# Performance work log

Hardware: AMD Instinct MI355X
Metric: run time of the kernel (lower is better)

## Reference

```python
import math
import jax, jax.numpy as jnp
import numpy as np

NL, D, H, V, L = 6, 512, 8, 32000, 512
DK = D // H
PAD = 1


def _ln(x, g, b, eps=1e-6):
    mu = jnp.mean(x, -1, keepdims=True)
    var = jnp.mean((x - mu) ** 2, -1, keepdims=True)
    return (x - mu) * jax.lax.rsqrt(var + eps) * g + b


def _mha(xq, xkv, w, b, mask):
    # w: [4, D, D] (q, k, v, out), b: [4, D]; mask True = disallowed
    B, Tq, _ = xq.shape
    Tk = xkv.shape[1]
    q = (xq @ w[0] + b[0]).reshape(B, Tq, H, DK).transpose(0, 2, 1, 3)
    k = (xkv @ w[1] + b[1]).reshape(B, Tk, H, DK).transpose(0, 2, 1, 3)
    v = (xkv @ w[2] + b[2]).reshape(B, Tk, H, DK).transpose(0, 2, 1, 3)
    s = jnp.einsum('bhqd,bhkd->bhqk', q, k) / math.sqrt(DK)
    s = jnp.where(mask, -jnp.inf, s)
    a = jax.nn.softmax(s, -1)
    o = jnp.einsum('bhqk,bhkd->bhqd', a, v).transpose(0, 2, 1, 3).reshape(B, Tq, D)
    return o @ w[3] + b[3]


def _ffn(x, w1, b1, w2, b2):
    return jnp.maximum(x @ w1 + b1, 0.0) @ w2 + b2


def _forward(src, tgt, tok_emb, pos_emb, enc_attn_w, enc_attn_b, enc_ffn_w1, enc_ffn_b1,
             enc_ffn_w2, enc_ffn_b2, enc_ln, enc_fln, dec_attn_w, dec_attn_b,
             dec_ffn_w1, dec_ffn_b1, dec_ffn_w2, dec_ffn_b2, dec_ln, dec_fln):
    B, S = src.shape
    T = tgt.shape[1]
    src_mask = (src == PAD)[:, None, None, :]                    # [B,1,1,S]
    causal = ~jnp.tril(jnp.ones((T, T), bool))
    trg_mask = causal[None, None] | (tgt == PAD)[:, None, None, :]  # [B,1,T,T]

    # ----- encoder (pre-LN sublayers with residual) -----
    x = tok_emb[src] + pos_emb[jnp.arange(S)]
    for i in range(NL):
        h = _ln(x, enc_ln[i, 0, 0], enc_ln[i, 0, 1])
        x = x + _mha(h, h, enc_attn_w[i], enc_attn_b[i], src_mask)
        h = _ln(x, enc_ln[i, 1, 0], enc_ln[i, 1, 1])
        x = x + _ffn(h, enc_ffn_w1[i], enc_ffn_b1[i], enc_ffn_w2[i], enc_ffn_b2[i])
    mem = _ln(x, enc_fln[0], enc_fln[1])

    # ----- decoder -----
    y = tok_emb[tgt] + pos_emb[jnp.arange(T)]
    for i in range(NL):
        h = _ln(y, dec_ln[i, 0, 0], dec_ln[i, 0, 1])
        y = y + _mha(h, h, dec_attn_w[i, :4], dec_attn_b[i, :4], trg_mask)
        h = _ln(y, dec_ln[i, 1, 0], dec_ln[i, 1, 1])
        y = y + _mha(h, mem, dec_attn_w[i, 4:], dec_attn_b[i, 4:], src_mask)
        h = _ln(y, dec_ln[i, 2, 0], dec_ln[i, 2, 1])
        y = y + _ffn(h, dec_ffn_w1[i], dec_ffn_b1[i], dec_ffn_w2[i], dec_ffn_b2[i])
    y = _ln(y, dec_fln[0], dec_fln[1])

    # Generator: tied-weight projection + log_softmax
    logits = y @ tok_emb.T                                       # [B,T,V]
    return jax.nn.log_softmax(logits, -1)


def setup_inputs() -> dict:
    key = jax.random.key(0)
    ks = jax.random.split(key, 12)
    n = lambda k, shape, s=0.02: jax.random.normal(k, shape, jnp.float32) * s
    B, S, T = 8, 128, 128
    ln2 = jnp.tile(jnp.stack([jnp.ones(D), jnp.zeros(D)])[None, None], (NL, 2, 1, 1))
    ln3 = jnp.tile(jnp.stack([jnp.ones(D), jnp.zeros(D)])[None, None], (NL, 3, 1, 1))
    fln = jnp.stack([jnp.ones(D), jnp.zeros(D)])
    return {
        'src': jax.random.randint(ks[0], (B, S), 2, V),
        'tgt': jax.random.randint(ks[1], (B, T), 2, V),
        'tok_emb': n(ks[2], (V, D)),
        'pos_emb': n(ks[3], (L, D)),
        'enc_attn_w': n(ks[4], (NL, 4, D, D)),
        'enc_attn_b': jnp.zeros((NL, 4, D)),
        'enc_ffn_w1': n(ks[5], (NL, D, 4 * D)),
        'enc_ffn_b1': jnp.zeros((NL, 4 * D)),
        'enc_ffn_w2': n(ks[6], (NL, 4 * D, D)),
        'enc_ffn_b2': jnp.zeros((NL, D)),
        'enc_ln': ln2,
        'enc_fln': fln,
        'dec_attn_w': n(ks[7], (NL, 8, D, D)),
        'dec_attn_b': jnp.zeros((NL, 8, D)),
        'dec_ffn_w1': n(ks[8], (NL, D, 4 * D)),
        'dec_ffn_b1': jnp.zeros((NL, 4 * D)),
        'dec_ffn_w2': n(ks[9], (NL, 4 * D, D)),
        'dec_ffn_b2': jnp.zeros((NL, D)),
        'dec_ln': ln3,
        'dec_fln': fln,
    }


def reference(src, tgt, tok_emb, pos_emb, enc_attn_w, enc_attn_b, enc_ffn_w1, enc_ffn_b1,
              enc_ffn_w2, enc_ffn_b2, enc_ln, enc_fln, dec_attn_w, dec_attn_b,
              dec_ffn_w1, dec_ffn_b1, dec_ffn_w2, dec_ffn_b2, dec_ln, dec_fln):
    return _forward(src, tgt, tok_emb, pos_emb, enc_attn_w, enc_attn_b, enc_ffn_w1,
                    enc_ffn_b1, enc_ffn_w2, enc_ffn_b2, enc_ln, enc_fln, dec_attn_w,
                    dec_attn_b, dec_ffn_w1, dec_ffn_b1, dec_ffn_w2, dec_ffn_b2,
                    dec_ln, dec_fln)
```

## Files before the change

### kernel.cpp

```cpp
#include <hip/hip_runtime.h>
#include <hip/hip_bf16.h>

typedef unsigned short u16;
typedef unsigned int u32;
typedef __attribute__((ext_vector_type(8))) short bf8_t;
typedef __attribute__((ext_vector_type(4))) float f4_t;

#define D 512
#define H 8
#define DK 64
#define NL 6
#define V 32000
#define FF 2048
#define B 8
#define S 128
#define NTOK (B * S)

static __device__ inline u16 f2bs(float x) {
    __hip_bfloat16 h = __float2bfloat16(x);
    return *reinterpret_cast<u16*>(&h);
}
static __device__ inline float blo(u32 u) { return __uint_as_float(u << 16); }
static __device__ inline float bhi(u32 u) { return __uint_as_float(u & 0xffff0000u); }
static __device__ inline u32 pk2(float a, float b) {
    return ((u32)f2bs(b) << 16) | f2bs(a);
}

__global__ __launch_bounds__(256) void wconv_t(const float* __restrict__ in,
                                               u16* __restrict__ out,
                                               int R, int C)
{
    __shared__ u16 T[32][40];
    const float* inz = in + (size_t)blockIdx.z * R * C;
    u16* outz = out + (size_t)blockIdx.z * R * C;
    int r0 = blockIdx.y * 32, c0 = blockIdx.x * 32;
    int tid = threadIdx.x;
    {
        int r = tid >> 3, c4 = (tid & 7) * 4;
        float4 f = *(const float4*)&inz[(size_t)(r0 + r) * C + c0 + c4];
        T[c4 + 0][r] = f2bs(f.x);
        T[c4 + 1][r] = f2bs(f.y);
        T[c4 + 2][r] = f2bs(f.z);
        T[c4 + 3][r] = f2bs(f.w);
    }
    __syncthreads();
    {
        int c = tid >> 3, r4 = (tid & 7) * 4;
        u32 lo = ((u32)T[c][r4 + 1] << 16) | T[c][r4 + 0];
        u32 hi = ((u32)T[c][r4 + 3] << 16) | T[c][r4 + 2];
        uint2 p; p.x = lo; p.y = hi;
        *(uint2*)&outz[(size_t)(c0 + c) * R + r0 + r4] = p;
    }
}

__global__ __launch_bounds__(256) void ec_kernel(const float* __restrict__ in,
                                                 u16* __restrict__ out)
{
    size_t i = ((size_t)blockIdx.x * 256 + threadIdx.x) * 4;
    float4 f = *(const float4*)&in[i];
    uint2 p;
    p.x = pk2(f.x, f.y);
    p.y = pk2(f.z, f.w);
    *(uint2*)&out[i] = p;
}

__global__ __launch_bounds__(256) void embed2_kernel(
    const int* __restrict__ src, const int* __restrict__ tgt,
    const float* __restrict__ tok, const float* __restrict__ pos,
    float* __restrict__ xe, float* __restrict__ xd)
{
    int row = blockIdx.x;
    const int* ids; float* X; int r;
    if (row < NTOK) { ids = src; X = xe; r = row; }
    else            { ids = tgt; X = xd; r = row - NTOK; }
    int s  = r & (S - 1);
    int id = ids[r];
    int d  = threadIdx.x * 2;
    float2 t = *(const float2*)&tok[(size_t)id * D + d];
    float2 p = *(const float2*)&pos[(size_t)s * D + d];
    float2 o; o.x = t.x + p.x; o.y = t.y + p.y;
    *(float2*)&X[(size_t)r * D + d] = o;
}

__global__ void ln_kernel(const float* __restrict__ X,
                          const float* __restrict__ g,
                          const float* __restrict__ bta,
                          u16* __restrict__ Y)
{
    int row  = blockIdx.x;
    int lane = threadIdx.x;
    float v[8];
    float sum = 0.f;
#pragma unroll
    for (int i = 0; i < 8; ++i) {
        v[i] = X[row * D + i * 64 + lane];
        sum += v[i];
    }
#pragma unroll
    for (int off = 32; off > 0; off >>= 1) sum += __shfl_xor(sum, off);
    float mu = sum * (1.f / D);
    float var = 0.f;
#pragma unroll
    for (int i = 0; i < 8; ++i) { float d = v[i] - mu; var += d * d; }
#pragma unroll
    for (int off = 32; off > 0; off >>= 1) var += __shfl_xor(var, off);
    var *= (1.f / D);
    float r = rsqrtf(var + 1e-6f);
#pragma unroll
    for (int i = 0; i < 8; ++i) {
        int d = i * 64 + lane;
        Y[row * D + d] = f2bs((v[i] - mu) * r * g[d] + bta[d]);
    }
}

template<int MT, int KC, int LNA>
__global__ __launch_bounds__(256) void gk(
    const u16* __restrict__ Abf, const float* __restrict__ Axf,
    const float* __restrict__ g, const float* __restrict__ be,
    const u16* __restrict__ Bt, const float* __restrict__ bias,
    const float* __restrict__ resid, void* __restrict__ Cout,
    int K, int N, int relu, int obf, int swz,
    long wzs, long bzs, long ozs)
{
    constexpr int THREADS = 256;
    constexpr int SL = KC / 8;
    constexpr int NA = MT * SL / THREADS;
    constexpr int NB = 64 * SL / THREADS;
    constexpr int NJ = (MT == 32) ? 2 : 4;
    constexpr int TPR = THREADS / MT;
    __shared__ __align__(16) u16 As[MT][KC + 8];
    __shared__ __align__(16) u16 Bs[64][KC + 8];
    __shared__ float muS[MT], rsS[MT];
    __shared__ float gS[LNA ? D : 4], beS[LNA ? D : 4];

    int tid = threadIdx.x;
    int col0, row0, z;
    if (swz) {
        int id = blockIdx.x;
        int s = id & 7, t = id >> 3;
        int r = t & 15, q = t >> 4;
        int c = q * 8 + s;
        if (c >= 500) return;
        col0 = c * 64; row0 = r * MT; z = 0;
    } else {
        col0 = blockIdx.x * 64; row0 = blockIdx.y * MT; z = blockIdx.z;
    }

    const float* bz = bias ? bias + (size_t)z * bzs : nullptr;
    const u16* Bz = Bt + (size_t)z * wzs;

    int wv  = tid >> 6, ln = tid & 63;
    int m16 = ln & 15, quad = ln >> 4;
    int rb  = (MT == 32) ? (wv & 1) * 16 : wv * 16;
    int cb  = (MT == 32) ? (wv >> 1) * 32 : 0;

    bf8_t  pA[LNA ? 1 : NA];
    float4 pAf[LNA ? 2 * NA : 1];
    bf8_t  pB[NB];

    auto loadA = [&](int kc) {
#pragma unroll
        for (int i = 0; i < NA; ++i) {
            int idx = tid + i * THREADS;
            int m = idx / SL, s8 = (idx % SL) * 8;
            if constexpr (LNA) {
                const float* sp = &Axf[(size_t)(row0 + m) * D + kc + s8];
                pAf[2 * i]     = *(const float4*)sp;
                pAf[2 * i + 1] = *(const float4*)(sp + 4);
            } else {
                pA[i] = *(const bf8_t*)&Abf[(size_t)(row0 + m) * K + kc + s8];
            }
        }
    };
    auto loadB = [&](int kc) {
#pragma unroll
        for (int i = 0; i < NB; ++i) {
            int idx = tid + i * THREADS;
            int n = idx / SL, s8 = (idx % SL) * 8;
            pB[i] = *(const bf8_t*)&Bz[(size_t)(col0 + n) * K + kc + s8];
        }
    };
    auto writeLDS = [&](int kc) {
#pragma unroll
        for (int i = 0; i < NA; ++i) {
            int idx = tid + i * THREADS;
            int m = idx / SL, s8 = (idx % SL) * 8;
            if constexpr (LNA) {
                float mu = muS[m], rs = rsS[m];
                float4 f0 = pAf[2 * i], f1 = pAf[2 * i + 1];
                float4 g0 = *(const float4*)&gS[kc + s8];
                float4 g1 = *(const float4*)&gS[kc + s8 + 4];
                float4 b0 = *(const float4*)&beS[kc + s8];
                float4 b1 = *(const float4*)&beS[kc + s8 + 4];
                uint4 o;
                o.x = pk2((f0.x - mu) * rs * g0.x + b0.x, (f0.y - mu) * rs * g0.y + b0.y);
                o.y = pk2((f0.z - mu) * rs * g0.z + b0.z, (f0.w - mu) * rs * g0.w + b0.w);
                o.z = pk2((f1.x - mu) * rs * g1.x + b1.x, (f1.y - mu) * rs * g1.y + b1.y);
                o.w = pk2((f1.z - mu) * rs * g1.z + b1.z, (f1.w - mu) * rs * g1.w + b1.w);
                *(uint4*)&As[m][s8] = o;
            } else {
                *(bf8_t*)&As[m][s8] = pA[i];
            }
        }
#pragma unroll
        for (int i = 0; i < NB; ++i) {
            int idx = tid + i * THREADS;
            int n = idx / SL, s8 = (idx % SL) * 8;
            *(bf8_t*)&Bs[n][s8] = pB[i];
        }
    };

    loadA(0);
    loadB(0);
    if constexpr (LNA) {
        if (tid < 128) *(float4*)&gS[tid * 4] = *(const float4*)&g[tid * 4];
        else           *(float4*)&beS[(tid - 128) * 4] = *(const float4*)&be[(tid - 128) * 4];
        int r = tid / TPR, sR = tid % TPR;
        const float* xr = Axf + (size_t)(row0 + r) * D;
        float sum = 0.f, ss = 0.f;
#pragma unroll
        for (int c = 0; c < D / (TPR * 4); ++c) {
            float4 f = *(const float4*)&xr[c * TPR * 4 + sR * 4];
            sum += f.x + f.y + f.z + f.w;
            ss  += f.x * f.x + f.y * f.y + f.z * f.z + f.w * f.w;
        }
#pragma unroll
        for (int o = 1; o < TPR; o <<= 1) {
            sum += __shfl_xor(sum, o);
            ss  += __shfl_xor(ss, o);
        }
        if (sR == 0) {
            float mu  = sum * (1.f / D);
            float var = ss * (1.f / D) - mu * mu;
            muS[r] = mu;
            rsS[r] = rsqrtf(var + 1e-6f);
        }
        __syncthreads();
    }

    f4_t acc[NJ];
#pragma unroll
    for (int j = 0; j < NJ; ++j) acc[j] = (f4_t){0.f, 0.f, 0.f, 0.f};

    for (int kc = 0; kc < K; kc += KC) {
        writeLDS(kc);
        __syncthreads();
        if (kc + KC < K) { loadA(kc + KC); loadB(kc + KC); }
#pragma unroll
        for (int ks = 0; ks < KC / 32; ++ks) {
            bf8_t a = *(const bf8_t*)&As[rb + m16][ks * 32 + quad * 8];
#pragma unroll
            for (int j = 0; j < NJ; ++j) {
                bf8_t b = *(const bf8_t*)&Bs[cb + j * 16 + m16][ks * 32 + quad * 8];
                acc[j] = __builtin_amdgcn_mfma_f32_16x16x32_bf16(a, b, acc[j], 0, 0, 0);
            }
        }
        __syncthreads();
    }

#pragma unroll
    for (int j = 0; j < NJ; ++j) {
        int col = col0 + cb + j * 16 + m16;
        float bv = bz ? bz[col] : 0.f;
#pragma unroll
        for (int r = 0; r < 4; ++r) {
            int row = row0 + rb + quad * 4 + r;
            float val = acc[j][r] + bv;
            if (resid) val += resid[(size_t)row * N + col];
            if (relu) val = fmaxf(val, 0.f);
            if (obf) ((u16*)Cout + (size_t)z * ozs)[(size_t)row * N + col] = f2bs(val);
            else     ((float*)Cout + (size_t)z * ozs)[(size_t)row * N + col] = val;
        }
    }
}

__global__ __launch_bounds__(256) void attn_kernel(
    const u16* __restrict__ Qb, const u16* __restrict__ Kb,
    const u16* __restrict__ Vb, u16* __restrict__ Ob,
    const int* __restrict__ mask_ids, int causal)
{
    __shared__ u16 Ks[128][66];
    __shared__ u32 Vp[128][36];
    __shared__ u16 Qs[32][66];
    __shared__ float es[4][132];

    int qc = blockIdx.x;
    int h  = blockIdx.y;
    int b  = blockIdx.z;
    int tid = threadIdx.x;

    for (int i = tid; i < 1024; i += 256) {
        int t = i >> 3, d8 = (i & 7) * 8;
        size_t src = (size_t)(b * S + t) * D + h * DK + d8;
        uint4 kv = *(const uint4*)&Kb[src];
        *(u32*)&Ks[t][d8 + 0] = kv.x;
        *(u32*)&Ks[t][d8 + 2] = kv.y;
        *(u32*)&Ks[t][d8 + 4] = kv.z;
        *(u32*)&Ks[t][d8 + 6] = kv.w;
        uint4 vv = *(const uint4*)&Vb[src];
        *(uint4*)&Vp[t][d8 >> 1] = vv;
    }
    {
        int m = tid >> 3, d8 = (tid & 7) * 8;
        uint4 qv = *(const uint4*)&Qb[(size_t)(b * S + qc * 32 + m) * D + h * DK + d8];
        *(u32*)&Qs[m][d8 + 0] = qv.x;
        *(u32*)&Qs[m][d8 + 2] = qv.y;
        *(u32*)&Qs[m][d8 + 4] = qv.z;
        *(u32*)&Qs[m][d8 + 6] = qv.w;
    }
    __syncthreads();

    int w      = tid >> 6;
    int lane   = tid & 63;
    int d2     = lane & 31;
    int th     = lane >> 5;
    bool pad0  = (mask_ids[b * S + lane] == 1);
    bool pad1  = (mask_ids[b * S + 64 + lane] == 1);

    for (int qi = 0; qi < 8; ++qi) {
        int qloc = w * 8 + qi;
        int qpos = qc * 32 + qloc;

        float s0 = 0.f, s1 = 0.f;
#pragma unroll
        for (int i = 0; i < 32; ++i) {
            u32 qu = *(const u32*)&Qs[qloc][2 * i];
            u32 k0 = *(const u32*)&Ks[lane][2 * i];
            u32 k1 = *(const u32*)&Ks[lane + 64][2 * i];
            float ql = blo(qu), qh = bhi(qu);
            s0 += ql * blo(k0) + qh * bhi(k0);
            s1 += ql * blo(k1) + qh * bhi(k1);
        }
        s0 *= 0.125f; s1 *= 0.125f;
        if (pad0 || (causal && lane > qpos))        s0 = -1e30f;
        if (pad1 || (causal && (lane + 64) > qpos)) s1 = -1e30f;

        float mx = fmaxf(s0, s1);
#pragma unroll
        for (int off = 32; off > 0; off >>= 1) mx = fmaxf(mx, __shfl_xor(mx, off));
        float e0 = __expf(s0 - mx), e1 = __expf(s1 - mx);
        float l = e0 + e1;
#pragma unroll
        for (int off = 32; off > 0; off >>= 1) l += __shfl_xor(l, off);
        float inv = 1.f / l;
        es[w][lane]      = e0 * inv;
        es[w][lane + 64] = e1 * inv;

        float o0 = 0.f, o1 = 0.f;
#pragma unroll 8
        for (int i = 0; i < 64; ++i) {
            int t = th * 64 + i;
            float e = es[w][t];
            u32 vu = Vp[t][d2];
            o0 += e * blo(vu);
            o1 += e * bhi(vu);
        }
        o0 += __shfl_xor(o0, 32);
        o1 += __shfl_xor(o1, 32);
        if (th == 0) {
            u32 packed = ((u32)f2bs(o1) << 16) | f2bs(o0);
            *(u32*)&Ob[(size_t)(b * S + qpos) * D + h * DK + 2 * d2] = packed;
        }
    }
}

__global__ __launch_bounds__(256) void lsm_kernel(float* __restrict__ out)
{
    __shared__ float red[8];
    int row = blockIdx.x, tid = threadIdx.x;
    float* rp = out + (size_t)row * V;
    float v[125];
    float m = -1e30f;
#pragma unroll
    for (int i = 0; i < 125; ++i) {
        v[i] = rp[i * 256 + tid];
        m = fmaxf(m, v[i]);
    }
#pragma unroll
    for (int off = 32; off > 0; off >>= 1) m = fmaxf(m, __shfl_xor(m, off));
    int wv = tid >> 6;
    if ((tid & 63) == 0) red[wv] = m;
    __syncthreads();
    m = fmaxf(fmaxf(red[0], red[1]), fmaxf(red[2], red[3]));
    float l = 0.f;
#pragma unroll
    for (int i = 0; i < 125; ++i) l += __expf(v[i] - m);
#pragma unroll
    for (int off = 32; off > 0; off >>= 1) l += __shfl_xor(l, off);
    if ((tid & 63) == 0) red[4 + wv] = l;
    __syncthreads();
    l = (red[4] + red[5]) + (red[6] + red[7]);
    float c = m + logf(l);
#pragma unroll
    for (int i = 0; i < 125; ++i) rp[i * 256 + tid] = v[i] - c;
}

extern "C" void kernel_launch(void* const* d_in, const int* in_sizes, int n_in,
                              void* d_out, int out_size, void* d_ws, size_t ws_size,
                              hipStream_t stream)
{
    const int*   src        = (const int*)d_in[0];
    const int*   tgt        = (const int*)d_in[1];
    const float* tok_emb    = (const float*)d_in[2];
    const float* pos_emb    = (const float*)d_in[3];
    const float* enc_attn_w = (const float*)d_in[4];
    const float* enc_attn_b = (const float*)d_in[5];
    const float* enc_ffn_w1 = (const float*)d_in[6];
    const float* enc_ffn_b1 = (const float*)d_in[7];
    const float* enc_ffn_w2 = (const float*)d_in[8];
    const float* enc_ffn_b2 = (const float*)d_in[9];
    const float* enc_ln     = (const float*)d_in[10];
    const float* enc_fln    = (const float*)d_in[11];
    const float* dec_attn_w = (const float*)d_in[12];
    const float* dec_attn_b = (const float*)d_in[13];
    const float* dec_ffn_w1 = (const float*)d_in[14];
    const float* dec_ffn_b1 = (const float*)d_in[15];
    const float* dec_ffn_w2 = (const float*)d_in[16];
    const float* dec_ffn_b2 = (const float*)d_in[17];
    const float* dec_ln     = (const float*)d_in[18];
    const float* dec_fln    = (const float*)d_in[19];
    float* out = (float*)d_out;

    const size_t TOKD = (size_t)NTOK * D;
    const size_t DD   = (size_t)D * D;
    const size_t DF   = (size_t)D * FF;

    char* p = (char*)d_ws;
    auto carve = [&](size_t bytes) {
        void* r = (void*)p;
        p += (bytes + 255) & ~(size_t)255;
        return r;
    };
    u16* wtEA  = (u16*)carve(24 * DD * 2);
    u16* wtEF1 = (u16*)carve(6 * DF * 2);
    u16* wtEF2 = (u16*)carve(6 * DF * 2);
    u16* wtDA  = (u16*)carve(48 * DD * 2);
    u16* wtDF1 = (u16*)carve(6 * DF * 2);
    u16* wtDF2 = (u16*)carve(6 * DF * 2);
    u16* emb16 = (u16*)carve((size_t)V * D * 2);
    float* xe  = (float*)carve(TOKD * 4);
    float* xd  = (float*)carve(TOKD * 4);
    u16* h16   = (u16*)carve(TOKD * 2);
    u16* q16   = (u16*)carve(TOKD * 2 * 3);
    u16* k16   = q16 + TOKD;
    u16* v16   = k16 + TOKD;
    u16* ao16  = (u16*)carve(TOKD * 2);
    u16* mem16 = (u16*)carve(TOKD * 2);
    u16* mid16 = (u16*)carve((size_t)NTOK * FF * 2);
    u16* kc16  = (u16*)carve(6 * TOKD * 2);
    u16* vc16  = (u16*)carve(6 * TOKD * 2);

    dim3 b256(256), b64(64);
    dim3 gQKV(8, 32, 3);
    dim3 gP  (8, 32, 1);
    dim3 gKV6(8, 32, 6);
    dim3 gF1 (32, 16, 1);
    dim3 gF2 (8, 32, 1);
    dim3 gGen(8064, 1, 1);
    dim3 gAttn(4, H, B);

    wconv_t<<<dim3(16, 16, 24), b256, 0, stream>>>(enc_attn_w, wtEA, 512, 512);
    wconv_t<<<dim3(64, 16, 6),  b256, 0, stream>>>(enc_ffn_w1, wtEF1, 512, 2048);
    wconv_t<<<dim3(16, 64, 6),  b256, 0, stream>>>(enc_ffn_w2, wtEF2, 2048, 512);
    wconv_t<<<dim3(16, 16, 48), b256, 0, stream>>>(dec_attn_w, wtDA, 512, 512);
    wconv_t<<<dim3(64, 16, 6),  b256, 0, stream>>>(dec_ffn_w1, wtDF1, 512, 2048);
    wconv_t<<<dim3(16, 64, 6),  b256, 0, stream>>>(dec_ffn_w2, wtDF2, 2048, 512);
    ec_kernel<<<16000, b256, 0, stream>>>(tok_emb, emb16);

    embed2_kernel<<<2 * NTOK, b256, 0, stream>>>(src, tgt, tok_emb, pos_emb, xe, xd);

    for (int i = 0; i < NL; ++i) {
        const float* bb  = enc_attn_b + (size_t)i * 4 * D;
        const float* ln0 = enc_ln + (size_t)((i * 2 + 0) * 2) * D;
        const float* ln1 = enc_ln + (size_t)((i * 2 + 1) * 2) * D;

        gk<32, 128, 1><<<gQKV, b256, 0, stream>>>(nullptr, xe, ln0, ln0 + D,
            wtEA + (size_t)i * 4 * DD, bb, nullptr, q16,
            512, 512, 0, 1, 0, (long)DD, (long)D, (long)TOKD);
        attn_kernel<<<gAttn, b256, 0, stream>>>(q16, k16, v16, ao16, src, 0);
        gk<32, 128, 0><<<gP, b256, 0, stream>>>(ao16, nullptr, nullptr, nullptr,
            wtEA + (size_t)(i * 4 + 3) * DD, bb + 3 * D, xe, xe,
            512, 512, 0, 0, 0, 0, 0, 0);
        gk<64, 128, 1><<<gF1, b256, 0, stream>>>(nullptr, xe, ln1, ln1 + D,
            wtEF1 + (size_t)i * DF, enc_ffn_b1 + (size_t)i * FF, nullptr, mid16,
            512, 2048, 1, 1, 0, 0, 0, 0);
        gk<32, 128, 0><<<gF2, b256, 0, stream>>>(mid16, nullptr, nullptr, nullptr,
            wtEF2 + (size_t)i * DF, enc_ffn_b2 + (size_t)i * D, xe, xe,
            2048, 512, 0, 0, 0, 0, 0, 0);
    }
    ln_kernel<<<NTOK, b64, 0, stream>>>(xe, enc_fln, enc_fln + D, mem16);

    gk<32, 128, 0><<<gKV6, b256, 0, stream>>>(mem16, nullptr, nullptr, nullptr,
        wtDA + 5 * DD, dec_attn_b + 5 * D, nullptr, kc16,
        512, 512, 0, 1, 0, (long)(8 * DD), (long)(8 * D), (long)TOKD);
    gk<32, 128, 0><<<gKV6, b256, 0, stream>>>(mem16, nullptr, nullptr, nullptr,
        wtDA + 6 * DD, dec_attn_b + 6 * D, nullptr, vc16,
        512, 512, 0, 1, 0, (long)(8 * DD), (long)(8 * D), (long)TOKD);

    for (int i = 0; i < NL; ++i) {
        const float* bb  = dec_attn_b + (size_t)i * 8 * D;
        const u16*   wt  = wtDA + (size_t)i * 8 * DD;
        const float* ln0 = dec_ln + (size_t)((i * 3 + 0) * 2) * D;
        const float* ln1 = dec_ln + (size_t)((i * 3 + 1) * 2) * D;
        const float* ln2 = dec_ln + (size_t)((i * 3 + 2) * 2) * D;

        gk<32, 128, 1><<<gQKV, b256, 0, stream>>>(nullptr, xd, ln0, ln0 + D,
            wt, bb, nullptr, q16,
            512, 512, 0, 1, 0, (long)DD, (long)D, (long)TOKD);
        attn_kernel<<<gAttn, b256, 0, stream>>>(q16, k16, v16, ao16, tgt, 1);
        gk<32, 128, 0><<<gP, b256, 0, stream>>>(ao16, nullptr, nullptr, nullptr,
            wt + 3 * DD, bb + 3 * D, xd, xd,
            512, 512, 0, 0, 0, 0, 0, 0);

        gk<32, 128, 1><<<gP, b256, 0, stream>>>(nullptr, xd, ln1, ln1 + D,
            wt + 4 * DD, bb + 4 * D, nullptr, q16,
            512, 512, 0, 1, 0, 0, 0, 0);
        attn_kernel<<<gAttn, b256, 0, stream>>>(q16, kc16 + (size_t)i * TOKD,
            vc16 + (size_t)i * TOKD, ao16, src, 0);
        gk<32, 128, 0><<<gP, b256, 0, stream>>>(ao16, nullptr, nullptr, nullptr,
            wt + 7 * DD, bb + 7 * D, xd, xd,
            512, 512, 0, 0, 0, 0, 0, 0);

        gk<64, 128, 1><<<gF1, b256, 0, stream>>>(nullptr, xd, ln2, ln2 + D,
            wtDF1 + (size_t)i * DF, dec_ffn_b1 + (size_t)i * FF, nullptr, mid16,
            512, 2048, 1, 1, 0, 0, 0, 0);
        gk<32, 128, 0><<<gF2, b256, 0, stream>>>(mid16, nullptr, nullptr, nullptr,
            wtDF2 + (size_t)i * DF, dec_ffn_b2 + (size_t)i * D, xd, xd,
            2048, 512, 0, 0, 0, 0, 0, 0);
    }
    ln_kernel<<<NTOK, b64, 0, stream>>>(xd, dec_fln, dec_fln + D, h16);

    gk<64, 128, 0><<<gGen, b256, 0, stream>>>(h16, nullptr, nullptr, nullptr,
        emb16, nullptr, nullptr, out,
        512, V, 0, 0, 1, 0, 0, 0);
    lsm_kernel<<<NTOK, b256, 0, stream>>>(out);
}
```

Baseline: 1.687 ms.

## Fuse LN+QKV projection into attention, merge prep kernels, stage fp32 epilogue

Merges the six weight-conversion launches, embedding cast and embed kernels into one prep launch. Replaces the separate LN+QKV GEMM and attention kernels with fused kernels (fqa for self-attention, fca for cross-attention) that compute per-head Q/K/V in LDS and run attention directly, so the q/k/v tensors never go through global memory. Adds an LDS-staged, float4-coalesced fp32 epilogue to the GEMM and changes the generator GEMM K-chunk from 128 to 64. The fused kernels recompute K/V for every query-chunk block (4x redundant projection work) and use 512-thread blocks with large shared memory, which can lower occupancy.

Measured after the change: 1.600 ms. 1.05x faster.

```diff
diff --git a/kernel.cpp b/kernel.cpp
--- a/kernel.cpp
+++ b/kernel.cpp
@@ -26,15 +26,13 @@
     return ((u32)f2bs(b) << 16) | f2bs(a);
 }
 
-__global__ __launch_bounds__(256) void wconv_t(const float* __restrict__ in,
-                                               u16* __restrict__ out,
-                                               int R, int C)
+__device__ inline void wconv_body(const float* __restrict__ in, u16* __restrict__ out,
+                                  int R, int C, int bx, int by, int bz, int tid,
+                                  u16 (*T)[40])
 {
-    __shared__ u16 T[32][40];
-    const float* inz = in + (size_t)blockIdx.z * R * C;
-    u16* outz = out + (size_t)blockIdx.z * R * C;
-    int r0 = blockIdx.y * 32, c0 = blockIdx.x * 32;
-    int tid = threadIdx.x;
+    const float* inz = in + (size_t)bz * R * C;
+    u16* outz = out + (size_t)bz * R * C;
+    int r0 = by * 32, c0 = bx * 32;
     {
         int r = tid >> 3, c4 = (tid & 7) * 4;
         float4 f = *(const float4*)&inz[(size_t)(r0 + r) * C + c0 + c4];
@@ -53,33 +51,52 @@
     }
 }
 
-__global__ __launch_bounds__(256) void ec_kernel(const float* __restrict__ in,
-                                                 u16* __restrict__ out)
+__global__ __launch_bounds__(256) void prep(
+    const float* __restrict__ eaw, const float* __restrict__ ef1,
+    const float* __restrict__ ef2, const float* __restrict__ daw,
+    const float* __restrict__ df1, const float* __restrict__ df2,
+    u16* __restrict__ wEA, u16* __restrict__ wEF1, u16* __restrict__ wEF2,
+    u16* __restrict__ wDA, u16* __restrict__ wDF1, u16* __restrict__ wDF2,
+    const float* __restrict__ tok, u16* __restrict__ emb16,
+    const int* __restrict__ src, const int* __restrict__ tgt,
+    const float* __restrict__ pos, float* __restrict__ xe, float* __restrict__ xd)
 {
-    size_t i = ((size_t)blockIdx.x * 256 + threadIdx.x) * 4;
-    float4 f = *(const float4*)&in[i];
-    uint2 p;
-    p.x = pk2(f.x, f.y);
-    p.y = pk2(f.z, f.w);
-    *(uint2*)&out[i] = p;
-}
-
-__global__ __launch_bounds__(256) void embed2_kernel(
-    const int* __restrict__ src, const int* __restrict__ tgt,
-    const float* __restrict__ tok, const float* __restrict__ pos,
-    float* __restrict__ xe, float* __restrict__ xd)
-{
-    int row = blockIdx.x;
-    const int* ids; float* X; int r;
-    if (row < NTOK) { ids = src; X = xe; r = row; }
-    else            { ids = tgt; X = xd; r = row - NTOK; }
-    int s  = r & (S - 1);
-    int id = ids[r];
-    int d  = threadIdx.x * 2;
-    float2 t = *(const float2*)&tok[(size_t)id * D + d];
-    float2 p = *(const float2*)&pos[(size_t)s * D + d];
-    float2 o; o.x = t.x + p.x; o.y = t.y + p.y;
-    *(float2*)&X[(size_t)r * D + d] = o;
+    __shared__ u16 T[32][40];
+    int id = blockIdx.x, tid = threadIdx.x;
+    if (id < 6144)  { wconv_body(eaw, wEA, 512, 512,  id % 16, (id / 16) % 16, id / 256,  tid, T); return; }
+    id -= 6144;
+    if (id < 6144)  { wconv_body(ef1, wEF1, 512, 2048, id % 64, (id / 64) % 16, id / 1024, tid, T); return; }
+    id -= 6144;
+    if (id < 6144)  { wconv_body(ef2, wEF2, 2048, 512, id % 16, (id / 16) % 64, id / 1024, tid, T); return; }
+    id -= 6144;
+    if (id < 12288) { wconv_body(daw, wDA, 512, 512,  id % 16, (id / 16) % 16, id / 256,  tid, T); return; }
+    id -= 12288;
+    if (id < 6144)  { wconv_body(df1, wDF1, 512, 2048, id % 64, (id / 64) % 16, id / 1024, tid, T); return; }
+    id -= 6144;
+    if (id < 6144)  { wconv_body(df2, wDF2, 2048, 512, id % 16, (id / 16) % 64, id / 1024, tid, T); return; }
+    id -= 6144;
+    if (id < 16000) {
+        size_t i = ((size_t)id * 256 + tid) * 4;
+        float4 f = *(const float4*)&tok[i];
+        uint2 p;
+        p.x = pk2(f.x, f.y);
+        p.y = pk2(f.z, f.w);
+        *(uint2*)&emb16[i] = p;
+        return;
+    }
+    id -= 16000;
+    {
+        const int* ids; float* X; int r;
+        if (id < NTOK) { ids = src; X = xe; r = id; }
+        else           { ids = tgt; X = xd; r = id - NTOK; }
+        int s  = r & (S - 1);
+        int tk = ids[r];
+        int d  = tid * 2;
+        float2 t = *(const float2*)&tok[(size_t)tk * D + d];
+        float2 p = *(const float2*)&pos[(size_t)s * D + d];
+        float2 o; o.x = t.x + p.x; o.y = t.y + p.y;
+        *(float2*)&X[(size_t)r * D + d] = o;
+    }
 }
 
 __global__ void ln_kernel(const float* __restrict__ X,
@@ -128,8 +145,9 @@
     constexpr int NB = 64 * SL / THREADS;
     constexpr int NJ = (MT == 32) ? 2 : 4;
     constexpr int TPR = THREADS / MT;
-    __shared__ __align__(16) u16 As[MT][KC + 8];
-    __shared__ __align__(16) u16 Bs[64][KC + 8];
+    __shared__ __align__(16) u16 AB[(MT + 64) * (KC + 8)];
+    u16 (*As)[KC + 8] = (u16(*)[KC + 8])AB;
+    u16 (*Bs)[KC + 8] = (u16(*)[KC + 8])&AB[MT * (KC + 8)];
     __shared__ float muS[MT], rsS[MT];
     __shared__ float gS[LNA ? D : 4], beS[LNA ? D : 4];
 
@@ -258,38 +276,311 @@
         __syncthreads();
     }
 
-#pragma unroll
-    for (int j = 0; j < NJ; ++j) {
-        int col = col0 + cb + j * 16 + m16;
-        float bv = bz ? bz[col] : 0.f;
-#pragma unroll
-        for (int r = 0; r < 4; ++r) {
-            int row = row0 + rb + quad * 4 + r;
-            float val = acc[j][r] + bv;
-            if (resid) val += resid[(size_t)row * N + col];
-            if (relu) val = fmaxf(val, 0.f);
-            if (obf) ((u16*)Cout + (size_t)z * ozs)[(size_t)row * N + col] = f2bs(val);
-            else     ((float*)Cout + (size_t)z * ozs)[(size_t)row * N + col] = val;
-        }
-    }
-}
-
-__global__ __launch_bounds__(256) void attn_kernel(
-    const u16* __restrict__ Qb, const u16* __restrict__ Kb,
-    const u16* __restrict__ Vb, u16* __restrict__ Ob,
+    if (obf) {
+#pragma unroll
+        for (int j = 0; j < NJ; ++j) {
+            int col = col0 + cb + j * 16 + m16;
+            float bv = bz ? bz[col] : 0.f;
+#pragma unroll
+            for (int r = 0; r < 4; ++r) {
+                int row = row0 + rb + quad * 4 + r;
+                float val = acc[j][r] + bv;
+                if (relu) val = fmaxf(val, 0.f);
+                ((u16*)Cout + (size_t)z * ozs)[(size_t)row * N + col] = f2bs(val);
+            }
+        }
+    } else {
+        float (*Cs)[68] = (float(*)[68])AB;
+#pragma unroll
+        for (int j = 0; j < NJ; ++j)
+#pragma unroll
+            for (int r = 0; r < 4; ++r)
+                Cs[rb + quad * 4 + r][cb + j * 16 + m16] = acc[j][r];
+        __syncthreads();
+        float* Co = (float*)Cout + (size_t)z * ozs;
+#pragma unroll
+        for (int i = 0; i < MT / 16; ++i) {
+            int flat = (i * 256 + tid) * 4;
+            int row = flat >> 6, col = flat & 63;
+            float4 v = *(const float4*)&Cs[row][col];
+            if (bz) {
+                float4 b4 = *(const float4*)&bz[col0 + col];
+                v.x += b4.x; v.y += b4.y; v.z += b4.z; v.w += b4.w;
+            }
+            if (resid) {
+                float4 r4 = *(const float4*)&resid[(size_t)(row0 + row) * N + col0 + col];
+                v.x += r4.x; v.y += r4.y; v.z += r4.z; v.w += r4.w;
+            }
+            if (relu) {
+                v.x = fmaxf(v.x, 0.f); v.y = fmaxf(v.y, 0.f);
+                v.z = fmaxf(v.z, 0.f); v.w = fmaxf(v.w, 0.f);
+            }
+            *(float4*)&Co[(size_t)(row0 + row) * N + col0 + col] = v;
+        }
+    }
+}
+
+__global__ __launch_bounds__(512) void fqa(
+    const float* __restrict__ X, const float* __restrict__ g,
+    const float* __restrict__ be, const u16* __restrict__ W,
+    const float* __restrict__ bb, u16* __restrict__ Ob,
     const int* __restrict__ mask_ids, int causal)
 {
+    __shared__ __align__(16) u16 As[128][72];
+    __shared__ __align__(16) u16 Ws[3][64][72];
     __shared__ u16 Ks[128][66];
     __shared__ u32 Vp[128][36];
     __shared__ u16 Qs[32][66];
-    __shared__ float es[4][132];
-
-    int qc = blockIdx.x;
-    int h  = blockIdx.y;
-    int b  = blockIdx.z;
+    __shared__ float es[8][132];
+    __shared__ float muS[128], rsS[128];
+    __shared__ float gS[D], beS[D];
+
+    int qc = blockIdx.x, h = blockIdx.y, b = blockIdx.z;
     int tid = threadIdx.x;
-
-    for (int i = tid; i < 1024; i += 256) {
+    int w = tid >> 6, lane = tid & 63;
+    int m16 = lane & 15, quad = lane >> 4;
+    const float* Xb = X + (size_t)(b * S) * D;
+    const size_t DDs = (size_t)D * D;
+
+    float4 pAf[4];
+    bf8_t  pW[3];
+    auto loadA = [&](int kc) {
+#pragma unroll
+        for (int i = 0; i < 2; ++i) {
+            int idx = tid + i * 512;
+            int m = idx >> 3, s8 = (idx & 7) * 8;
+            const float* sp = &Xb[(size_t)m * D + kc + s8];
+            pAf[2 * i]     = *(const float4*)sp;
+            pAf[2 * i + 1] = *(const float4*)(sp + 4);
+        }
+    };
+    auto loadW = [&](int kc) {
+        int n = tid >> 3, s8 = (tid & 7) * 8;
+#pragma unroll
+        for (int m = 0; m < 3; ++m)
+            pW[m] = *(const bf8_t*)&W[m * DDs + (size_t)(h * 64 + n) * D + kc + s8];
+    };
+    auto writeLDS = [&](int kc) {
+#pragma unroll
+        for (int i = 0; i < 2; ++i) {
+            int idx = tid + i * 512;
+            int m = idx >> 3, s8 = (idx & 7) * 8;
+            float mu = muS[m], rs = rsS[m];
+            float4 f0 = pAf[2 * i], f1 = pAf[2 * i + 1];
+            float4 g0 = *(const float4*)&gS[kc + s8];
+            float4 g1 = *(const float4*)&gS[kc + s8 + 4];
+            float4 b0 = *(const float4*)&beS[kc + s8];
+            float4 b1 = *(const float4*)&beS[kc + s8 + 4];
+            uint4 o;
+            o.x = pk2((f0.x - mu) * rs * g0.x + b0.x, (f0.y - mu) * rs * g0.y + b0.y);
+            o.y = pk2((f0.z - mu) * rs * g0.z + b0.z, (f0.w - mu) * rs * g0.w + b0.w);
+            o.z = pk2((f1.x - mu) * rs * g1.x + b1.x, (f1.y - mu) * rs * g1.y + b1.y);
+            o.w = pk2((f1.z - mu) * rs * g1.z + b1.z, (f1.w - mu) * rs * g1.w + b1.w);
+            *(uint4*)&As[m][s8] = o;
+        }
+        {
+            int n = tid >> 3, s8 = (tid & 7) * 8;
+#pragma unroll
+            for (int m = 0; m < 3; ++m)
+                *(bf8_t*)&Ws[m][n][s8] = pW[m];
+        }
+    };
+
+    loadA(0);
+    loadW(0);
+    if (tid < 128)      *(float4*)&gS[tid * 4] = *(const float4*)&g[tid * 4];
+    else if (tid < 256) *(float4*)&beS[(tid - 128) * 4] = *(const float4*)&be[(tid - 128) * 4];
+    {
+        int r = tid >> 2, sub = tid & 3;
+        const float* xr = Xb + (size_t)r * D + sub * 128;
+        float sum = 0.f, ss = 0.f;
+#pragma unroll
+        for (int c = 0; c < 32; ++c) {
+            float4 f = *(const float4*)&xr[c * 4];
+            sum += f.x + f.y + f.z + f.w;
+            ss  += f.x * f.x + f.y * f.y + f.z * f.z + f.w * f.w;
+        }
+        sum += __shfl_xor(sum, 1); sum += __shfl_xor(sum, 2);
+        ss  += __shfl_xor(ss, 1);  ss  += __shfl_xor(ss, 2);
+        if (sub == 0) {
+            float mu  = sum * (1.f / D);
+            float var = ss * (1.f / D) - mu * mu;
+            muS[r] = mu;
+            rsS[r] = rsqrtf(var + 1e-6f);
+        }
+    }
+    __syncthreads();
+
+    f4_t accK[4], accV[4], accQ;
+#pragma unroll
+    for (int j = 0; j < 4; ++j) {
+        accK[j] = (f4_t){0.f, 0.f, 0.f, 0.f};
+        accV[j] = (f4_t){0.f, 0.f, 0.f, 0.f};
+    }
+    accQ = (f4_t){0.f, 0.f, 0.f, 0.f};
+
+    for (int kc = 0; kc < 512; kc += 64) {
+        writeLDS(kc);
+        __syncthreads();
+        if (kc < 448) { loadA(kc + 64); loadW(kc + 64); }
+#pragma unroll
+        for (int ks = 0; ks < 2; ++ks) {
+            int ko = ks * 32 + quad * 8;
+            bf8_t akv = *(const bf8_t*)&As[w * 16 + m16][ko];
+            bf8_t aq  = *(const bf8_t*)&As[qc * 32 + (w & 1) * 16 + m16][ko];
+#pragma unroll
+            for (int j = 0; j < 4; ++j) {
+                bf8_t bk = *(const bf8_t*)&Ws[1][j * 16 + m16][ko];
+                accK[j] = __builtin_amdgcn_mfma_f32_16x16x32_bf16(akv, bk, accK[j], 0, 0, 0);
+                bf8_t bv = *(const bf8_t*)&Ws[2][j * 16 + m16][ko];
+                accV[j] = __builtin_amdgcn_mfma_f32_16x16x32_bf16(akv, bv, accV[j], 0, 0, 0);
+            }
+            bf8_t bq = *(const bf8_t*)&Ws[0][(w >> 1) * 16 + m16][ko];
+            accQ = __builtin_amdgcn_mfma_f32_16x16x32_bf16(aq, bq, accQ, 0, 0, 0);
+        }
+        __syncthreads();
+    }
+
+    {
+        const float* bq = bb + h * 64;
+        const float* bk = bb + D + h * 64;
+        const float* bv = bb + 2 * D + h * 64;
+#pragma unroll
+        for (int j = 0; j < 4; ++j) {
+            int col = j * 16 + m16;
+            float bkv = bk[col], bvv = bv[col];
+#pragma unroll
+            for (int r = 0; r < 4; ++r) {
+                int row = w * 16 + quad * 4 + r;
+                Ks[row][col] = f2bs(accK[j][r] + bkv);
+                float vv = accV[j][r] + bvv;
+                float vo = __shfl_xor(vv, 1);
+                if ((m16 & 1) == 0)
+                    Vp[row][j * 8 + (m16 >> 1)] = pk2(vv, vo);
+            }
+        }
+        {
+            int col = (w >> 1) * 16 + m16;
+            float bqv = bq[col];
+#pragma unroll
+            for (int r = 0; r < 4; ++r)
+                Qs[(w & 1) * 16 + quad * 4 + r][col] = f2bs(accQ[r] + bqv);
+        }
+    }
+    __syncthreads();
+
+    int d2 = lane & 31, th = lane >> 5;
+    bool pad0 = (mask_ids[b * S + lane] == 1);
+    bool pad1 = (mask_ids[b * S + 64 + lane] == 1);
+
+    for (int qi = 0; qi < 4; ++qi) {
+        int qloc = w * 4 + qi;
+        int qpos = qc * 32 + qloc;
+
+        float s0 = 0.f, s1 = 0.f;
+#pragma unroll
+        for (int i = 0; i < 32; ++i) {
+            u32 qu = *(const u32*)&Qs[qloc][2 * i];
+            u32 k0 = *(const u32*)&Ks[lane][2 * i];
+            u32 k1 = *(const u32*)&Ks[lane + 64][2 * i];
+            float ql = blo(qu), qh = bhi(qu);
+            s0 += ql * blo(k0) + qh * bhi(k0);
+            s1 += ql * blo(k1) + qh * bhi(k1);
+        }
+        s0 *= 0.125f; s1 *= 0.125f;
+        if (pad0 || (causal && lane > qpos))        s0 = -1e30f;
+        if (pad1 || (causal && (lane + 64) > qpos)) s1 = -1e30f;
+
+        float mx = fmaxf(s0, s1);
+#pragma unroll
+        for (int off = 32; off > 0; off >>= 1) mx = fmaxf(mx, __shfl_xor(mx, off));
+        float e0 = __expf(s0 - mx), e1 = __expf(s1 - mx);
+        float l = e0 + e1;
+#pragma unroll
+        for (int off = 32; off > 0; off >>= 1) l += __shfl_xor(l, off);
+        float inv = 1.f / l;
+        es[w][lane]      = e0 * inv;
+        es[w][lane + 64] = e1 * inv;
+
+        float o0 = 0.f, o1 = 0.f;
+#pragma unroll 8
+        for (int i = 0; i < 64; ++i) {
+            int t = th * 64 + i;
+            float e = es[w][t];
+            u32 vu = Vp[t][d2];
+            o0 += e * blo(vu);
+            o1 += e * bhi(vu);
+        }
+        o0 += __shfl_xor(o0, 32);
+        o1 += __shfl_xor(o1, 32);
+        if (th == 0) {
+            u32 packed = ((u32)f2bs(o1) << 16) | f2bs(o0);
+            *(u32*)&Ob[(size_t)(b * S + qpos) * D + h * DK + 2 * d2] = packed;
+        }
+    }
+}
+
+__global__ __launch_bounds__(512) void fca(
+    const float* __restrict__ X, const float* __restrict__ g,
+    const float* __restrict__ be, const u16* __restrict__ Wq,
+    const float* __restrict__ bq, const u16* __restrict__ Kb,
+    const u16* __restrict__ Vb, u16* __restrict__ Ob,
+    const int* __restrict__ mask_ids)
+{
+    __shared__ __align__(16) u16 As[32][72];
+    __shared__ __align__(16) u16 Wqs[64][72];
+    __shared__ u16 Ks[128][66];
+    __shared__ u32 Vp[128][36];
+    __shared__ u16 Qs[32][66];
+    __shared__ float es[8][132];
+    __shared__ float muS[32], rsS[32];
+    __shared__ float gS[D], beS[D];
+
+    int qc = blockIdx.x, h = blockIdx.y, b = blockIdx.z;
+    int tid = threadIdx.x;
+    int w = tid >> 6, lane = tid & 63;
+    int m16 = lane & 15, quad = lane >> 4;
+    const float* Xb = X + (size_t)(b * S + qc * 32) * D;
+
+    float4 pAf[2];
+    bf8_t  pW;
+    auto loadA = [&](int kc) {
+        if (tid < 256) {
+            int m = tid >> 3, s8 = (tid & 7) * 8;
+            const float* sp = &Xb[(size_t)m * D + kc + s8];
+            pAf[0] = *(const float4*)sp;
+            pAf[1] = *(const float4*)(sp + 4);
+        }
+    };
+    auto loadW = [&](int kc) {
+        int n = tid >> 3, s8 = (tid & 7) * 8;
+        pW = *(const bf8_t*)&Wq[(size_t)(h * 64 + n) * D + kc + s8];
+    };
+    auto writeLDS = [&](int kc) {
+        if (tid < 256) {
+            int m = tid >> 3, s8 = (tid & 7) * 8;
+            float mu = muS[m], rs = rsS[m];
+            float4 f0 = pAf[0], f1 = pAf[1];
+            float4 g0 = *(const float4*)&gS[kc + s8];
+            float4 g1 = *(const float4*)&gS[kc + s8 + 4];
+            float4 b0 = *(const float4*)&beS[kc + s8];
+            float4 b1 = *(const float4*)&beS[kc + s8 + 4];
+            uint4 o;
+            o.x = pk2((f0.x - mu) * rs * g0.x + b0.x, (f0.y - mu) * rs * g0.y + b0.y);
+            o.y = pk2((f0.z - mu) * rs * g0.z + b0.z, (f0.w - mu) * rs * g0.w + b0.w);
+            o.z = pk2((f1.x - mu) * rs * g1.x + b1.x, (f1.y - mu) * rs * g1.y + b1.y);
+            o.w = pk2((f1.z - mu) * rs * g1.z + b1.z, (f1.w - mu) * rs * g1.w + b1.w);
+            *(uint4*)&As[m][s8] = o;
+        }
+        {
+            int n = tid >> 3, s8 = (tid & 7) * 8;
+            *(bf8_t*)&Wqs[n][s8] = pW;
+        }
+    };
+
+    loadA(0);
+    loadW(0);
+    for (int i = tid; i < 1024; i += 512) {
         int t = i >> 3, d8 = (i & 7) * 8;
         size_t src = (size_t)(b * S + t) * D + h * DK + d8;
         uint4 kv = *(const uint4*)&Kb[src];
@@ -300,25 +591,61 @@
         uint4 vv = *(const uint4*)&Vb[src];
         *(uint4*)&Vp[t][d8 >> 1] = vv;
     }
+    if (tid < 128)      *(float4*)&gS[tid * 4] = *(const float4*)&g[tid * 4];
+    else if (tid < 256) *(float4*)&beS[(tid - 128) * 4] = *(const float4*)&be[(tid - 128) * 4];
     {
-        int m = tid >> 3, d8 = (tid & 7) * 8;
-        uint4 qv = *(const uint4*)&Qb[(size_t)(b * S + qc * 32 + m) * D + h * DK + d8];
-        *(u32*)&Qs[m][d8 + 0] = qv.x;
-        *(u32*)&Qs[m][d8 + 2] = qv.y;
-        *(u32*)&Qs[m][d8 + 4] = qv.z;
-        *(u32*)&Qs[m][d8 + 6] = qv.w;
+        int r = tid >> 4, sub = tid & 15;
+        const float* xr = Xb + (size_t)r * D + sub * 32;
+        float sum = 0.f, ss = 0.f;
+#pragma unroll
+        for (int c = 0; c < 8; ++c) {
+            float4 f = *(const float4*)&xr[c * 4];
+            sum += f.x + f.y + f.z + f.w;
+            ss  += f.x * f.x + f.y * f.y + f.z * f.z + f.w * f.w;
+        }
+#pragma unroll
+        for (int o = 1; o < 16; o <<= 1) {
+            sum += __shfl_xor(sum, o);
+            ss  += __shfl_xor(ss, o);
+        }
+        if (sub == 0) {
+            float mu  = sum * (1.f / D);
+            float var = ss * (1.f / D) - mu * mu;
+            muS[r] = mu;
+            rsS[r] = rsqrtf(var + 1e-6f);
+        }
     }
     __syncthreads();
 
-    int w      = tid >> 6;
-    int lane   = tid & 63;
-    int d2     = lane & 31;
-    int th     = lane >> 5;
-    bool pad0  = (mask_ids[b * S + lane] == 1);
-    bool pad1  = (mask_ids[b * S + 64 + lane] == 1);
-
-    for (int qi = 0; qi < 8; ++qi) {
-        int qloc = w * 8 + qi;
+    f4_t accQ = (f4_t){0.f, 0.f, 0.f, 0.f};
+    for (int kc = 0; kc < 512; kc += 64) {
+        writeLDS(kc);
+        __syncthreads();
+        if (kc < 448) { loadA(kc + 64); loadW(kc + 64); }
+#pragma unroll
+        for (int ks = 0; ks < 2; ++ks) {
+            int ko = ks * 32 + quad * 8;
+            bf8_t aq = *(const bf8_t*)&As[(w & 1) * 16 + m16][ko];
+            bf8_t bq2 = *(const bf8_t*)&Wqs[(w >> 1) * 16 + m16][ko];
+            accQ = __builtin_amdgcn_mfma_f32_16x16x32_bf16(aq, bq2, accQ, 0, 0, 0);
+        }
+        __syncthreads();
+    }
+    {
+        int col = (w >> 1) * 16 + m16;
+        float bqv = bq[h * 64 + col];
+#pragma unroll
+        for (int r = 0; r < 4; ++r)
+            Qs[(w & 1) * 16 + quad * 4 + r][col] = f2bs(accQ[r] + bqv);
+    }
+    __syncthreads();
+
+    int d2 = lane & 31, th = lane >> 5;
+    bool pad0 = (mask_ids[b * S + lane] == 1);
+    bool pad1 = (mask_ids[b * S + 64 + lane] == 1);
+
+    for (int qi = 0; qi < 4; ++qi) {
+        int qloc = w * 4 + qi;
         int qpos = qc * 32 + qloc;
 
         float s0 = 0.f, s1 = 0.f;
@@ -332,8 +659,8 @@
             s1 += ql * blo(k1) + qh * bhi(k1);
         }
         s0 *= 0.125f; s1 *= 0.125f;
-        if (pad0 || (causal && lane > qpos))        s0 = -1e30f;
-        if (pad1 || (causal && (lane + 64) > qpos)) s1 = -1e30f;
+        if (pad0) s0 = -1e30f;
+        if (pad1) s1 = -1e30f;
 
         float mx = fmaxf(s0, s1);
 #pragma unroll
@@ -441,17 +768,13 @@
     float* xe  = (float*)carve(TOKD * 4);
     float* xd  = (float*)carve(TOKD * 4);
     u16* h16   = (u16*)carve(TOKD * 2);
-    u16* q16   = (u16*)carve(TOKD * 2 * 3);
-    u16* k16   = q16 + TOKD;
-    u16* v16   = k16 + TOKD;
     u16* ao16  = (u16*)carve(TOKD * 2);
     u16* mem16 = (u16*)carve(TOKD * 2);
     u16* mid16 = (u16*)carve((size_t)NTOK * FF * 2);
     u16* kc16  = (u16*)carve(6 * TOKD * 2);
     u16* vc16  = (u16*)carve(6 * TOKD * 2);
 
-    dim3 b256(256), b64(64);
-    dim3 gQKV(8, 32, 3);
+    dim3 b256(256), b512(512), b64(64);
     dim3 gP  (8, 32, 1);
     dim3 gKV6(8, 32, 6);
     dim3 gF1 (32, 16, 1);
@@ -459,25 +782,18 @@
     dim3 gGen(8064, 1, 1);
     dim3 gAttn(4, H, B);
 
-    wconv_t<<<dim3(16, 16, 24), b256, 0, stream>>>(enc_attn_w, wtEA, 512, 512);
-    wconv_t<<<dim3(64, 16, 6),  b256, 0, stream>>>(enc_ffn_w1, wtEF1, 512, 2048);
-    wconv_t<<<dim3(16, 64, 6),  b256, 0, stream>>>(enc_ffn_w2, wtEF2, 2048, 512);
-    wconv_t<<<dim3(16, 16, 48), b256, 0, stream>>>(dec_attn_w, wtDA, 512, 512);
-    wconv_t<<<dim3(64, 16, 6),  b256, 0, stream>>>(dec_ffn_w1, wtDF1, 512, 2048);
-    wconv_t<<<dim3(16, 64, 6),  b256, 0, stream>>>(dec_ffn_w2, wtDF2, 2048, 512);
-    ec_kernel<<<16000, b256, 0, stream>>>(tok_emb, emb16);
-
-    embed2_kernel<<<2 * NTOK, b256, 0, stream>>>(src, tgt, tok_emb, pos_emb, xe, xd);
+    prep<<<61056, b256, 0, stream>>>(enc_attn_w, enc_ffn_w1, enc_ffn_w2,
+                                     dec_attn_w, dec_ffn_w1, dec_ffn_w2,
+                                     wtEA, wtEF1, wtEF2, wtDA, wtDF1, wtDF2,
+                                     tok_emb, emb16, src, tgt, pos_emb, xe, xd);
 
     for (int i = 0; i < NL; ++i) {
         const float* bb  = enc_attn_b + (size_t)i * 4 * D;
         const float* ln0 = enc_ln + (size_t)((i * 2 + 0) * 2) * D;
         const float* ln1 = enc_ln + (size_t)((i * 2 + 1) * 2) * D;
 
-        gk<32, 128, 1><<<gQKV, b256, 0, stream>>>(nullptr, xe, ln0, ln0 + D,
-            wtEA + (size_t)i * 4 * DD, bb, nullptr, q16,
-            512, 512, 0, 1, 0, (long)DD, (long)D, (long)TOKD);
-        attn_kernel<<<gAttn, b256, 0, stream>>>(q16, k16, v16, ao16, src, 0);
+        fqa<<<gAttn, b512, 0, stream>>>(xe, ln0, ln0 + D, wtEA + (size_t)i * 4 * DD,
+                                        bb, ao16, src, 0);
         gk<32, 128, 0><<<gP, b256, 0, stream>>>(ao16, nullptr, nullptr, nullptr,
             wtEA + (size_t)(i * 4 + 3) * DD, bb + 3 * D, xe, xe,
             512, 512, 0, 0, 0, 0, 0, 0);
@@ -504,19 +820,14 @@
         const float* ln1 = dec_ln + (size_t)((i * 3 + 1) * 2) * D;
         const float* ln2 = dec_ln + (size_t)((i * 3 + 2) * 2) * D;
 
-        gk<32, 128, 1><<<gQKV, b256, 0, stream>>>(nullptr, xd, ln0, ln0 + D,
-            wt, bb, nullptr, q16,
-            512, 512, 0, 1, 0, (long)DD, (long)D, (long)TOKD);
-        attn_kernel<<<gAttn, b256, 0, stream>>>(q16, k16, v16, ao16, tgt, 1);
+        fqa<<<gAttn, b512, 0, stream>>>(xd, ln0, ln0 + D, wt, bb, ao16, tgt, 1);
         gk<32, 128, 0><<<gP, b256, 0, stream>>>(ao16, nullptr, nullptr, nullptr,
             wt + 3 * DD, bb + 3 * D, xd, xd,
             512, 512, 0, 0, 0, 0, 0, 0);
 
-        gk<32, 128, 1><<<gP, b256, 0, stream>>>(nullptr, xd, ln1, ln1 + D,
-            wt + 4 * DD, bb + 4 * D, nullptr, q16,
-            512, 512, 0, 1, 0, 0, 0, 0);
-        attn_kernel<<<gAttn, b256, 0, stream>>>(q16, kc16 + (size_t)i * TOKD,
-            vc16 + (size_t)i * TOKD, ao16, src, 0);
+        fca<<<gAttn, b512, 0, stream>>>(xd, ln1, ln1 + D, wt + 4 * DD, bb + 4 * D,
+                                        kc16 + (size_t)i * TOKD, vc16 + (size_t)i * TOKD,
+                                        ao16, src);
         gk<32, 128, 0><<<gP, b256, 0, stream>>>(ao16, nullptr, nullptr, nullptr,
             wt + 7 * DD, bb + 7 * D, xd, xd,
             512, 512, 0, 0, 0, 0, 0, 0);
@@ -530,7 +841,7 @@
     }
     ln_kernel<<<NTOK, b64, 0, stream>>>(xd, dec_fln, dec_fln + D, h16);
 
-    gk<64, 128, 0><<<gGen, b256, 0, stream>>>(h16, nullptr, nullptr, nullptr,
+    gk<64, 64, 0><<<gGen, b256, 0, stream>>>(h16, nullptr, nullptr, nullptr,
         emb16, nullptr, nullptr, out,
         512, V, 0, 0, 1, 0, 0, 0);
     lsm_kernel<<<NTOK, b256, 0, stream>>>(out);
```
